# Performance work log

Hardware: AMD Instinct MI355X
Metric: run time of the kernel (lower is better)

The kernel has to match this reference:

```python
import jax, jax.numpy as jnp
import numpy as np

EPS = 1e-12  # F.normalize default eps


def _normalize(x):
    # F.normalize(x): x / max(||x||_2 over dim=1, eps)
    n = jnp.sqrt(jnp.sum(x * x, axis=1, keepdims=True))
    return x / jnp.maximum(n, EPS)


def _layer_loss(t, s, n):
    d = (_normalize(t) - _normalize(s)) ** 2
    # np.percentile(., 99.9) with linear interpolation == jnp.quantile(., 0.999);
    # torch version detaches (cpu numpy), so stop_gradient matches semantics.
    dhard = jax.lax.stop_gradient(jnp.quantile(d.reshape(-1), 0.999))
    mask = d >= dhard
    cnt = jnp.sum(mask).astype(d.dtype)
    hard_mean = jnp.sum(jnp.where(mask, d, 0.0)) / cnt
    return hard_mean + jnp.mean(n * n)


def setup_inputs() -> dict:
    key = jax.random.key(0)
    shapes = {
        't1': (16, 64, 128, 128), 's1': (16, 64, 128, 128), 'n1': (16, 64, 128, 128),
        't2': (16, 128, 64, 64),  's2': (16, 128, 64, 64),  'n2': (16, 128, 64, 64),
        't3': (16, 256, 32, 32),  's3': (16, 256, 32, 32),  'n3': (16, 256, 32, 32),
    }
    ks = jax.random.split(key, len(shapes))
    return {name: jax.random.normal(k, shp, dtype=jnp.float32)
            for k, (name, shp) in zip(ks, shapes.items())}


def reference(t1, s1, n1, t2, s2, n2, t3, s3, n3):
    losses = jnp.stack([
        _layer_loss(t1, s1, n1),
        _layer_loss(t2, s2, n2),
        _layer_loss(t3, s3, n3),
    ])
    return jnp.sum(losses)
```

## Files before the change

kernel.cpp:

```cpp
#include <hip/hip_runtime.h>

#define NBINS 4352
#define ACC_OFF (3 * NBINS)

typedef float    f4v __attribute__((ext_vector_type(4)));
typedef _Float16 h4v __attribute__((ext_vector_type(4)));

template<int C, int HWSHIFT, int PSHIFT, int LAYER>
__device__ __forceinline__ void hist_layer(
    const float* __restrict__ t, const float* __restrict__ s, const float* __restrict__ n,
    int lb, unsigned int* __restrict__ ws_u, float* __restrict__ ws_f,
    unsigned int* cnt_sh, float* inv_sh)
{
    const int HW  = 1 << HWSHIFT;
    const int P   = 1 << PSHIFT;
    const int NPQ = P >> 2;
    const int G   = 1024 / P;
    const int tid = threadIdx.x;
    const int w   = tid >> 6;
    const int l   = tid & 63;
    const int pq  = l & (NPQ - 1);
    const int cs  = l >> (PSHIFT - 2);

    const int p0 = lb << PSHIFT;
    const int b  = p0 >> HWSHIFT;
    const int q  = p0 & (HW - 1);
    const int c0 = w * (C / 4) + cs * 16;
    const size_t base = ((size_t)(b * C + c0) << HWSHIFT) + q + 4 * pq;

    const float* tp = t + base;
    const float* sp = s + base;
    const float* np = n + base;

    h4v th[16], sh[16];
    f4v accT = {0.f,0.f,0.f,0.f}, accS = {0.f,0.f,0.f,0.f};
    float aN = 0.f;

    #pragma unroll
    for (int k0 = 0; k0 < 16; k0 += 4) {
        f4v tt[4], ss[4], nn[4];
        #pragma unroll
        for (int u = 0; u < 4; ++u) {
            const size_t o = (size_t)(k0 + u) << HWSHIFT;
            tt[u] = __builtin_nontemporal_load((const f4v*)(tp + o));
            ss[u] = __builtin_nontemporal_load((const f4v*)(sp + o));
            nn[u] = __builtin_nontemporal_load((const f4v*)(np + o));
        }
        #pragma unroll
        for (int u = 0; u < 4; ++u) {
            accT += tt[u] * tt[u];
            accS += ss[u] * ss[u];
            aN += nn[u].x*nn[u].x + nn[u].y*nn[u].y + nn[u].z*nn[u].z + nn[u].w*nn[u].w;
            th[k0+u] = (h4v){(_Float16)tt[u].x, (_Float16)tt[u].y,
                             (_Float16)tt[u].z, (_Float16)tt[u].w};
            sh[k0+u] = (h4v){(_Float16)ss[u].x, (_Float16)ss[u].y,
                             (_Float16)ss[u].z, (_Float16)ss[u].w};
        }
    }

    float* ovT = (float*)cnt_sh;
    float* ovS = ovT + 1024;
    float* ovN = ovT + 2048;
    const int g = (w * (64 / NPQ)) + cs;
    ((f4v*)ovT)[g * NPQ + pq] = accT;
    ((f4v*)ovS)[g * NPQ + pq] = accS;
    #pragma unroll
    for (int o = 32; o > 0; o >>= 1) aN += __shfl_down(aN, o, 64);
    if (l == 0) ovN[w] = aN;
    __syncthreads();

    if (tid < P) {
        float nT = 0.f, nS = 0.f;
        #pragma unroll
        for (int gg = 0; gg < G; ++gg) { nT += ovT[gg * P + tid]; nS += ovS[gg * P + tid]; }
        inv_sh[tid]     = 1.0f / fmaxf(sqrtf(nT), 1e-12f);
        inv_sh[P + tid] = 1.0f / fmaxf(sqrtf(nS), 1e-12f);
    }
    if (tid == 0)
        atomicAdd(&ws_f[ACC_OFF + LAYER], ovN[0] + ovN[1] + ovN[2] + ovN[3]);
    __syncthreads();

    for (int i = tid; i < NBINS / 4; i += 256)
        ((uint4*)cnt_sh)[i] = make_uint4(0u, 0u, 0u, 0u);
    __syncthreads();

    f4v iT = ((const f4v*)inv_sh)[pq];
    f4v iS = ((const f4v*)(inv_sh + P))[pq];
    #pragma unroll
    for (int k = 0; k < 16; ++k) {
        f4v tv = {(float)th[k].x, (float)th[k].y, (float)th[k].z, (float)th[k].w};
        f4v sv = {(float)sh[k].x, (float)sh[k].y, (float)sh[k].z, (float)sh[k].w};
        f4v a  = tv * iT - sv * iS;
        f4v d  = a * a;
        unsigned b0 = min(__float_as_uint(d.x) >> 18, (unsigned)(NBINS - 1));
        unsigned b1 = min(__float_as_uint(d.y) >> 18, (unsigned)(NBINS - 1));
        unsigned b2 = min(__float_as_uint(d.z) >> 18, (unsigned)(NBINS - 1));
        unsigned b3 = min(__float_as_uint(d.w) >> 18, (unsigned)(NBINS - 1));
        atomicAdd(&cnt_sh[b0], 1u);
        atomicAdd(&cnt_sh[b1], 1u);
        atomicAdd(&cnt_sh[b2], 1u);
        atomicAdd(&cnt_sh[b3], 1u);
    }
    __syncthreads();

    unsigned int* gc = ws_u + LAYER * NBINS;
    for (int i = tid; i < NBINS; i += 256) {
        unsigned c = cnt_sh[i];
        if (c) atomicAdd(&gc[i], c);
    }
}

__global__ __launch_bounds__(256, 3) void stfpm_hist(
    const float* __restrict__ t0, const float* __restrict__ s0, const float* __restrict__ n0,
    const float* __restrict__ t1, const float* __restrict__ s1, const float* __restrict__ n1,
    const float* __restrict__ t2, const float* __restrict__ s2, const float* __restrict__ n2,
    unsigned int* __restrict__ ws_u, float* __restrict__ ws_f)
{
    __shared__ __align__(16) unsigned int cnt_sh[NBINS];
    __shared__ __align__(16) float inv_sh[512];
    const int bid = blockIdx.x;
    if (bid < 256)
        hist_layer<256, 10, 6, 2>(t2, s2, n2, bid,       ws_u, ws_f, cnt_sh, inv_sh);
    else if (bid < 768)
        hist_layer<128, 12, 7, 1>(t1, s1, n1, bid - 256, ws_u, ws_f, cnt_sh, inv_sh);
    else
        hist_layer<64,  14, 8, 0>(t0, s0, n0, bid - 768, ws_u, ws_f, cnt_sh, inv_sh);
}

__device__ __forceinline__ float bin_mid(int b) {
    float lo = __uint_as_float((unsigned)b << 18);
    float hi = __uint_as_float((unsigned)(b + 1) << 18);
    return 0.5f * (lo + hi);
}

__global__ __launch_bounds__(256) void stfpm_finalize(
    const unsigned int* __restrict__ ws_u, const float* __restrict__ ws_f,
    float* __restrict__ out)
{
    __shared__ unsigned int cchunk[256];
    __shared__ float        schunk[256];
    const int tid = threadIdx.x;

    const int   targets[3] = {16778, 8389, 4195};
    const float Ns[3]      = {16777216.f, 8388608.f, 4194304.f};
    const int   CHUNK = NBINS / 256;

    float total = 0.f;
    for (int layer = 0; layer < 3; ++layer) {
        const unsigned int* gc = ws_u + layer * NBINS;
        unsigned int c = 0; float sv = 0.f;
        const int b0 = tid * CHUNK;
        for (int i = 0; i < CHUNK; ++i) {
            unsigned cc = gc[b0 + i];
            c += cc;
            if (cc) sv += (float)cc * bin_mid(b0 + i);
        }
        __syncthreads();
        cchunk[tid] = c; schunk[tid] = sv;
        __syncthreads();
        if (tid == 0) {
            const int target = targets[layer];
            long long cum = 0; float sAbove = 0.f;
            int ch = 255;
            while (ch >= 0 && cum + (long long)cchunk[ch] < target) {
                cum += cchunk[ch]; sAbove += schunk[ch]; --ch;
            }
            int bin = ch * CHUNK + CHUNK - 1;
            while (bin >= ch * CHUNK && cum + (long long)gc[bin] < target) {
                unsigned cc = gc[bin];
                cum += cc; sAbove += (float)cc * bin_mid(bin); --bin;
            }
            unsigned cb = gc[bin];
            int j = target - (int)cum;
            float lo = __uint_as_float((unsigned)bin << 18);
            float hi = __uint_as_float((unsigned)(bin + 1) << 18);
            float wd = hi - lo;
            float f  = (float)j / (float)cb;
            float topmean = hi - f * wd * 0.5f;
            topmean = fminf(fmaxf(topmean, lo), hi);
            float hard   = (sAbove + topmean * (float)j) / (float)target;
            float n2mean = ws_f[ACC_OFF + layer] / Ns[layer];
            total += hard + n2mean;
        }
        __syncthreads();
    }
    if (tid == 0) out[0] = total;
}

extern "C" void kernel_launch(void* const* d_in, const int* in_sizes, int n_in,
                              void* d_out, int out_size, void* d_ws, size_t ws_size,
                              hipStream_t stream)
{
    const float* t0 = (const float*)d_in[0];
    const float* s0 = (const float*)d_in[1];
    const float* n0 = (const float*)d_in[2];
    const float* t1 = (const float*)d_in[3];
    const float* s1 = (const float*)d_in[4];
    const float* n1 = (const float*)d_in[5];
    const float* t2 = (const float*)d_in[6];
    const float* s2 = (const float*)d_in[7];
    const float* n2 = (const float*)d_in[8];

    hipMemsetAsync(d_ws, 0, (size_t)(ACC_OFF + 8) * 4, stream);

    stfpm_hist<<<1792, 256, 0, stream>>>(t0, s0, n0, t1, s1, n1, t2, s2, n2,
                                         (unsigned int*)d_ws, (float*)d_ws);
    stfpm_finalize<<<1, 256, 0, stream>>>((const unsigned int*)d_ws,
                                          (const float*)d_ws, (float*)d_out);
}
```

Before: 84.42 us.

## Split noise sum-of-squares into separate interleaved blocks and halve per-block pixel work

The noise tensor reduction moves out of the histogram blocks into dedicated blocks that interleave one-in-five with the t/s histogram blocks. Each t/s block now handles half as many pixels (8 channels per thread instead of 16), and the launch grows from 1792 to 4480 blocks with launch bounds raised to 4 blocks per CU. Loads drop the nontemporal hint, and the shared histogram is zeroed before the norm reduction instead of after it. The aim is more parallelism and shorter per-block critical paths. The cost is twice as many per-block histogram flushes into global atomics, plus extra shared-memory zeroing.

```diff
diff --git a/kernel.cpp b/kernel.cpp
--- a/kernel.cpp
+++ b/kernel.cpp
@@ -7,15 +7,15 @@
 typedef _Float16 h4v __attribute__((ext_vector_type(4)));
 
 template<int C, int HWSHIFT, int PSHIFT, int LAYER>
-__device__ __forceinline__ void hist_layer(
-    const float* __restrict__ t, const float* __restrict__ s, const float* __restrict__ n,
-    int lb, unsigned int* __restrict__ ws_u, float* __restrict__ ws_f,
-    unsigned int* cnt_sh, float* inv_sh)
+__device__ __forceinline__ void ts_block(
+    const float* __restrict__ t, const float* __restrict__ s,
+    int lb, unsigned int* __restrict__ ws_u,
+    unsigned int* cnt_sh, float* ov_sh, float* inv_sh)
 {
     const int HW  = 1 << HWSHIFT;
     const int P   = 1 << PSHIFT;
     const int NPQ = P >> 2;
-    const int G   = 1024 / P;
+    const int G   = 1024 >> PSHIFT;
     const int tid = threadIdx.x;
     const int w   = tid >> 6;
     const int l   = tid & 63;
@@ -25,81 +25,60 @@
     const int p0 = lb << PSHIFT;
     const int b  = p0 >> HWSHIFT;
     const int q  = p0 & (HW - 1);
-    const int c0 = w * (C / 4) + cs * 16;
+    const int c0 = w * (C / 4) + cs * 8;
     const size_t base = ((size_t)(b * C + c0) << HWSHIFT) + q + 4 * pq;
-
     const float* tp = t + base;
     const float* sp = s + base;
-    const float* np = n + base;
-
-    h4v th[16], sh[16];
-    f4v accT = {0.f,0.f,0.f,0.f}, accS = {0.f,0.f,0.f,0.f};
-    float aN = 0.f;
-
-    #pragma unroll
-    for (int k0 = 0; k0 < 16; k0 += 4) {
-        f4v tt[4], ss[4], nn[4];
-        #pragma unroll
-        for (int u = 0; u < 4; ++u) {
-            const size_t o = (size_t)(k0 + u) << HWSHIFT;
-            tt[u] = __builtin_nontemporal_load((const f4v*)(tp + o));
-            ss[u] = __builtin_nontemporal_load((const f4v*)(sp + o));
-            nn[u] = __builtin_nontemporal_load((const f4v*)(np + o));
-        }
-        #pragma unroll
-        for (int u = 0; u < 4; ++u) {
-            accT += tt[u] * tt[u];
-            accS += ss[u] * ss[u];
-            aN += nn[u].x*nn[u].x + nn[u].y*nn[u].y + nn[u].z*nn[u].z + nn[u].w*nn[u].w;
-            th[k0+u] = (h4v){(_Float16)tt[u].x, (_Float16)tt[u].y,
-                             (_Float16)tt[u].z, (_Float16)tt[u].w};
-            sh[k0+u] = (h4v){(_Float16)ss[u].x, (_Float16)ss[u].y,
-                             (_Float16)ss[u].z, (_Float16)ss[u].w};
-        }
-    }
-
-    float* ovT = (float*)cnt_sh;
-    float* ovS = ovT + 1024;
-    float* ovN = ovT + 2048;
-    const int g = (w * (64 / NPQ)) + cs;
-    ((f4v*)ovT)[g * NPQ + pq] = accT;
-    ((f4v*)ovS)[g * NPQ + pq] = accS;
-    #pragma unroll
-    for (int o = 32; o > 0; o >>= 1) aN += __shfl_down(aN, o, 64);
-    if (l == 0) ovN[w] = aN;
-    __syncthreads();
-
-    if (tid < P) {
-        float nT = 0.f, nS = 0.f;
-        #pragma unroll
-        for (int gg = 0; gg < G; ++gg) { nT += ovT[gg * P + tid]; nS += ovS[gg * P + tid]; }
-        inv_sh[tid]     = 1.0f / fmaxf(sqrtf(nT), 1e-12f);
-        inv_sh[P + tid] = 1.0f / fmaxf(sqrtf(nS), 1e-12f);
-    }
-    if (tid == 0)
-        atomicAdd(&ws_f[ACC_OFF + LAYER], ovN[0] + ovN[1] + ovN[2] + ovN[3]);
-    __syncthreads();
+
+    f4v tt[8], ss[8];
+    #pragma unroll
+    for (int k = 0; k < 8; ++k) {
+        const size_t o = (size_t)k << HWSHIFT;
+        tt[k] = *(const f4v*)(tp + o);
+        ss[k] = *(const f4v*)(sp + o);
+    }
 
     for (int i = tid; i < NBINS / 4; i += 256)
         ((uint4*)cnt_sh)[i] = make_uint4(0u, 0u, 0u, 0u);
+
+    f4v accT = {0.f,0.f,0.f,0.f}, accS = {0.f,0.f,0.f,0.f};
+    h4v th[8], sh[8];
+    #pragma unroll
+    for (int k = 0; k < 8; ++k) {
+        accT += tt[k] * tt[k];
+        accS += ss[k] * ss[k];
+        th[k] = (h4v){(_Float16)tt[k].x, (_Float16)tt[k].y,
+                      (_Float16)tt[k].z, (_Float16)tt[k].w};
+        sh[k] = (h4v){(_Float16)ss[k].x, (_Float16)ss[k].y,
+                      (_Float16)ss[k].z, (_Float16)ss[k].w};
+    }
+    const int g_id = w * (64 / NPQ) + cs;
+    ((f4v*)ov_sh)[g_id * NPQ + pq]          = accT;
+    ((f4v*)(ov_sh + 1024))[g_id * NPQ + pq] = accS;
     __syncthreads();
 
+    if (tid < 2 * P) {
+        const int pos = tid & (P - 1);
+        const float* src = ov_sh + (tid < P ? 0 : 1024);
+        float acc = 0.f;
+        #pragma unroll
+        for (int gg = 0; gg < G; ++gg) acc += src[gg * P + pos];
+        inv_sh[tid] = 1.0f / fmaxf(sqrtf(acc), 1e-12f);
+    }
+    __syncthreads();
+
     f4v iT = ((const f4v*)inv_sh)[pq];
-    f4v iS = ((const f4v*)(inv_sh + P))[pq];
-    #pragma unroll
-    for (int k = 0; k < 16; ++k) {
+    f4v iS = ((const f4v*)inv_sh)[NPQ + pq];
+    #pragma unroll
+    for (int k = 0; k < 8; ++k) {
         f4v tv = {(float)th[k].x, (float)th[k].y, (float)th[k].z, (float)th[k].w};
         f4v sv = {(float)sh[k].x, (float)sh[k].y, (float)sh[k].z, (float)sh[k].w};
         f4v a  = tv * iT - sv * iS;
         f4v d  = a * a;
-        unsigned b0 = min(__float_as_uint(d.x) >> 18, (unsigned)(NBINS - 1));
-        unsigned b1 = min(__float_as_uint(d.y) >> 18, (unsigned)(NBINS - 1));
-        unsigned b2 = min(__float_as_uint(d.z) >> 18, (unsigned)(NBINS - 1));
-        unsigned b3 = min(__float_as_uint(d.w) >> 18, (unsigned)(NBINS - 1));
-        atomicAdd(&cnt_sh[b0], 1u);
-        atomicAdd(&cnt_sh[b1], 1u);
-        atomicAdd(&cnt_sh[b2], 1u);
-        atomicAdd(&cnt_sh[b3], 1u);
+        atomicAdd(&cnt_sh[min(__float_as_uint(d.x) >> 18, (unsigned)(NBINS-1))], 1u);
+        atomicAdd(&cnt_sh[min(__float_as_uint(d.y) >> 18, (unsigned)(NBINS-1))], 1u);
+        atomicAdd(&cnt_sh[min(__float_as_uint(d.z) >> 18, (unsigned)(NBINS-1))], 1u);
+        atomicAdd(&cnt_sh[min(__float_as_uint(d.w) >> 18, (unsigned)(NBINS-1))], 1u);
     }
     __syncthreads();
 
@@ -110,21 +89,46 @@
     }
 }
 
-__global__ __launch_bounds__(256, 3) void stfpm_hist(
+__device__ __forceinline__ void n_block(
+    const float* __restrict__ n, int layer, int lb, float* __restrict__ ws_f)
+{
+    const f4v* p = (const f4v*)n + ((size_t)lb << 13) + threadIdx.x;
+    float a = 0.f;
+    #pragma unroll 8
+    for (int i = 0; i < 32; ++i) {
+        f4v v = p[i * 256];
+        a += v.x*v.x + v.y*v.y + v.z*v.z + v.w*v.w;
+    }
+    #pragma unroll
+    for (int o = 32; o > 0; o >>= 1) a += __shfl_down(a, o, 64);
+    if ((threadIdx.x & 63) == 0) atomicAdd(&ws_f[ACC_OFF + layer], a);
+}
+
+__global__ __launch_bounds__(256, 4) void stfpm_main(
     const float* __restrict__ t0, const float* __restrict__ s0, const float* __restrict__ n0,
     const float* __restrict__ t1, const float* __restrict__ s1, const float* __restrict__ n1,
     const float* __restrict__ t2, const float* __restrict__ s2, const float* __restrict__ n2,
     unsigned int* __restrict__ ws_u, float* __restrict__ ws_f)
 {
     __shared__ __align__(16) unsigned int cnt_sh[NBINS];
-    __shared__ __align__(16) float inv_sh[512];
+    __shared__ __align__(16) float ov_sh[2048];
+    __shared__ __align__(16) float inv_sh[256];
     const int bid = blockIdx.x;
-    if (bid < 256)
-        hist_layer<256, 10, 6, 2>(t2, s2, n2, bid,       ws_u, ws_f, cnt_sh, inv_sh);
-    else if (bid < 768)
-        hist_layer<128, 12, 7, 1>(t1, s1, n1, bid - 256, ws_u, ws_f, cnt_sh, inv_sh);
+    const int g = bid / 5;
+    const int r = bid - g * 5;
+    if (r == 4) {
+        if (g < 128)      n_block(n2, 2, g,       ws_f);
+        else if (g < 384) n_block(n1, 1, g - 128, ws_f);
+        else              n_block(n0, 0, g - 384, ws_f);
+        return;
+    }
+    const int ts = g * 4 + r;
+    if (ts < 512)
+        ts_block<256, 10, 5, 2>(t2, s2, ts,        ws_u, cnt_sh, ov_sh, inv_sh);
+    else if (ts < 1536)
+        ts_block<128, 12, 6, 1>(t1, s1, ts - 512,  ws_u, cnt_sh, ov_sh, inv_sh);
     else
-        hist_layer<64,  14, 8, 0>(t0, s0, n0, bid - 768, ws_u, ws_f, cnt_sh, inv_sh);
+        ts_block<64,  14, 7, 0>(t0, s0, ts - 1536, ws_u, cnt_sh, ov_sh, inv_sh);
 }
 
 __device__ __forceinline__ float bin_mid(int b) {
@@ -203,7 +207,7 @@
 
     hipMemsetAsync(d_ws, 0, (size_t)(ACC_OFF + 8) * 4, stream);
 
-    stfpm_hist<<<1792, 256, 0, stream>>>(t0, s0, n0, t1, s1, n1, t2, s2, n2,
+    stfpm_main<<<4480, 256, 0, stream>>>(t0, s0, n0, t1, s1, n1, t2, s2, n2,
                                          (unsigned int*)d_ws, (float*)d_ws);
     stfpm_finalize<<<1, 256, 0, stream>>>((const unsigned int*)d_ws,
                                           (const float*)d_ws, (float*)d_out);
```

Result: slower. 98.28 us (+16.4%).

## Fuse finalize into histogram kernel via last-block completion counter

Applied to the files above, without the earlier changes.

Removes the separate single-block finalize launch. Each block increments an agent-scope done counter after its global histogram flush, and the last block to finish runs the quantile and loss reduction using atomic loads. This saves one kernel launch and its gap, at the cost of an extra atomic and barrier per block. It also switches the t and s loads from nontemporal to ordinary loads, which changes cache behaviour. The bin-walk loop is also slightly restructured.

```diff
diff --git a/kernel.cpp b/kernel.cpp
--- a/kernel.cpp
+++ b/kernel.cpp
@@ -2,9 +2,72 @@
 
 #define NBINS 4352
 #define ACC_OFF (3 * NBINS)
+#define DONE_OFF (ACC_OFF + 4)
+#define NBLOCKS 1792
 
 typedef float    f4v __attribute__((ext_vector_type(4)));
 typedef _Float16 h4v __attribute__((ext_vector_type(4)));
+
+__device__ __forceinline__ float bin_lo(int b)  { return __uint_as_float((unsigned)b << 18); }
+__device__ __forceinline__ float bin_mid(int b) { return 0.5f * (bin_lo(b) + bin_lo(b + 1)); }
+
+__device__ __forceinline__ unsigned agent_load_u(const unsigned* p) {
+    return __hip_atomic_load(p, __ATOMIC_RELAXED, __HIP_MEMORY_SCOPE_AGENT);
+}
+__device__ __forceinline__ float agent_load_f(const float* p) {
+    return __hip_atomic_load(p, __ATOMIC_RELAXED, __HIP_MEMORY_SCOPE_AGENT);
+}
+
+__device__ void finalize_body(const unsigned* __restrict__ ws_u,
+                              const float* __restrict__ ws_f,
+                              float* __restrict__ out, unsigned* lds)
+{
+    unsigned* cchunk = lds;
+    float*    schunk = (float*)(lds + 256);
+    const int tid = threadIdx.x;
+    const int   targets[3] = {16778, 8389, 4195};
+    const float Ns[3]      = {16777216.f, 8388608.f, 4194304.f};
+    const int   CHUNK = NBINS / 256;
+
+    float total = 0.f;
+    for (int layer = 0; layer < 3; ++layer) {
+        const unsigned* gc = ws_u + layer * NBINS;
+        unsigned c = 0; float sv = 0.f;
+        const int b0 = tid * CHUNK;
+        for (int i = 0; i < CHUNK; ++i) {
+            unsigned cc = agent_load_u(gc + b0 + i);
+            c += cc;
+            if (cc) sv += (float)cc * bin_mid(b0 + i);
+        }
+        __syncthreads();
+        cchunk[tid] = c; schunk[tid] = sv;
+        __syncthreads();
+        if (tid == 0) {
+            const int target = targets[layer];
+            long long cum = 0; float sAbove = 0.f;
+            int ch = 255;
+            while (ch >= 0 && cum + (long long)cchunk[ch] < target) {
+                cum += cchunk[ch]; sAbove += schunk[ch]; --ch;
+            }
+            int bin = ch * CHUNK + CHUNK - 1;
+            unsigned cb = agent_load_u(gc + bin);
+            while (bin > ch * CHUNK && cum + (long long)cb < target) {
+                cum += cb; sAbove += (float)cb * bin_mid(bin);
+                --bin; cb = agent_load_u(gc + bin);
+            }
+            int j = target - (int)cum;
+            float lo = bin_lo(bin), hi = bin_lo(bin + 1);
+            float f  = (float)j / (float)cb;
+            float topmean = hi - f * (hi - lo) * 0.5f;
+            topmean = fminf(fmaxf(topmean, lo), hi);
+            float hard   = (sAbove + topmean * (float)j) / (float)target;
+            float n2mean = agent_load_f(ws_f + ACC_OFF + layer) / Ns[layer];
+            total += hard + n2mean;
+        }
+        __syncthreads();
+    }
+    if (tid == 0) out[0] = total;
+}
 
 template<int C, int HWSHIFT, int PSHIFT, int LAYER>
 __device__ __forceinline__ void hist_layer(
@@ -15,7 +78,7 @@
     const int HW  = 1 << HWSHIFT;
     const int P   = 1 << PSHIFT;
     const int NPQ = P >> 2;
-    const int G   = 1024 / P;
+    const int G   = 1024 >> PSHIFT;
     const int tid = threadIdx.x;
     const int w   = tid >> 6;
     const int l   = tid & 63;
@@ -42,8 +105,8 @@
         #pragma unroll
         for (int u = 0; u < 4; ++u) {
             const size_t o = (size_t)(k0 + u) << HWSHIFT;
-            tt[u] = __builtin_nontemporal_load((const f4v*)(tp + o));
-            ss[u] = __builtin_nontemporal_load((const f4v*)(sp + o));
+            tt[u] = *(const f4v*)(tp + o);
+            ss[u] = *(const f4v*)(sp + o);
             nn[u] = __builtin_nontemporal_load((const f4v*)(np + o));
         }
         #pragma unroll
@@ -110,14 +173,16 @@
     }
 }
 
-__global__ __launch_bounds__(256, 3) void stfpm_hist(
+__global__ __launch_bounds__(256, 3) void stfpm_main(
     const float* __restrict__ t0, const float* __restrict__ s0, const float* __restrict__ n0,
     const float* __restrict__ t1, const float* __restrict__ s1, const float* __restrict__ n1,
     const float* __restrict__ t2, const float* __restrict__ s2, const float* __restrict__ n2,
-    unsigned int* __restrict__ ws_u, float* __restrict__ ws_f)
+    unsigned int* __restrict__ ws_u, float* __restrict__ ws_f, float* __restrict__ out)
 {
     __shared__ __align__(16) unsigned int cnt_sh[NBINS];
     __shared__ __align__(16) float inv_sh[512];
+    __shared__ unsigned last_flag;
+
     const int bid = blockIdx.x;
     if (bid < 256)
         hist_layer<256, 10, 6, 2>(t2, s2, n2, bid,       ws_u, ws_f, cnt_sh, inv_sh);
@@ -125,66 +190,15 @@
         hist_layer<128, 12, 7, 1>(t1, s1, n1, bid - 256, ws_u, ws_f, cnt_sh, inv_sh);
     else
         hist_layer<64,  14, 8, 0>(t0, s0, n0, bid - 768, ws_u, ws_f, cnt_sh, inv_sh);
-}
-
-__device__ __forceinline__ float bin_mid(int b) {
-    float lo = __uint_as_float((unsigned)b << 18);
-    float hi = __uint_as_float((unsigned)(b + 1) << 18);
-    return 0.5f * (lo + hi);
-}
-
-__global__ __launch_bounds__(256) void stfpm_finalize(
-    const unsigned int* __restrict__ ws_u, const float* __restrict__ ws_f,
-    float* __restrict__ out)
-{
-    __shared__ unsigned int cchunk[256];
-    __shared__ float        schunk[256];
-    const int tid = threadIdx.x;
-
-    const int   targets[3] = {16778, 8389, 4195};
-    const float Ns[3]      = {16777216.f, 8388608.f, 4194304.f};
-    const int   CHUNK = NBINS / 256;
-
-    float total = 0.f;
-    for (int layer = 0; layer < 3; ++layer) {
-        const unsigned int* gc = ws_u + layer * NBINS;
-        unsigned int c = 0; float sv = 0.f;
-        const int b0 = tid * CHUNK;
-        for (int i = 0; i < CHUNK; ++i) {
-            unsigned cc = gc[b0 + i];
-            c += cc;
-            if (cc) sv += (float)cc * bin_mid(b0 + i);
-        }
-        __syncthreads();
-        cchunk[tid] = c; schunk[tid] = sv;
-        __syncthreads();
-        if (tid == 0) {
-            const int target = targets[layer];
-            long long cum = 0; float sAbove = 0.f;
-            int ch = 255;
-            while (ch >= 0 && cum + (long long)cchunk[ch] < target) {
-                cum += cchunk[ch]; sAbove += schunk[ch]; --ch;
-            }
-            int bin = ch * CHUNK + CHUNK - 1;
-            while (bin >= ch * CHUNK && cum + (long long)gc[bin] < target) {
-                unsigned cc = gc[bin];
-                cum += cc; sAbove += (float)cc * bin_mid(bin); --bin;
-            }
-            unsigned cb = gc[bin];
-            int j = target - (int)cum;
-            float lo = __uint_as_float((unsigned)bin << 18);
-            float hi = __uint_as_float((unsigned)(bin + 1) << 18);
-            float wd = hi - lo;
-            float f  = (float)j / (float)cb;
-            float topmean = hi - f * wd * 0.5f;
-            topmean = fminf(fmaxf(topmean, lo), hi);
-            float hard   = (sAbove + topmean * (float)j) / (float)target;
-            float n2mean = ws_f[ACC_OFF + layer] / Ns[layer];
-            total += hard + n2mean;
-        }
-        __syncthreads();
-    }
-    if (tid == 0) out[0] = total;
+
+    __syncthreads();
+    if (threadIdx.x == 0)
+        last_flag = (__hip_atomic_fetch_add(&ws_u[DONE_OFF], 1u,
+                         __ATOMIC_ACQ_REL, __HIP_MEMORY_SCOPE_AGENT)
+                     == (unsigned)(NBLOCKS - 1));
+    __syncthreads();
+    if (last_flag)
+        finalize_body(ws_u, ws_f, out, cnt_sh);
 }
 
 extern "C" void kernel_launch(void* const* d_in, const int* in_sizes, int n_in,
@@ -203,8 +217,7 @@
 
     hipMemsetAsync(d_ws, 0, (size_t)(ACC_OFF + 8) * 4, stream);
 
-    stfpm_hist<<<1792, 256, 0, stream>>>(t0, s0, n0, t1, s1, n1, t2, s2, n2,
-                                         (unsigned int*)d_ws, (float*)d_ws);
-    stfpm_finalize<<<1, 256, 0, stream>>>((const unsigned int*)d_ws,
-                                          (const float*)d_ws, (float*)d_out);
-}
+    stfpm_main<<<NBLOCKS, 256, 0, stream>>>(t0, s0, n0, t1, s1, n1, t2, s2, n2,
+                                            (unsigned int*)d_ws, (float*)d_ws,
+                                            (float*)d_out);
+}
```

Result: slower. 156.3 us (+85.2%).
